# Kernel tuning notes

Measured on AMD Instinct MI355X. Metric: run time of the kernel, lower is better.

The kernel has to match this reference:

```python
import jax, jax.numpy as jnp
import numpy as np

N = 50000
E = 800000
HID = 32
HEADS = 8
OUT_DIM = 16
NEG_SLOPE = 0.2
LN_EPS = 1e-5


def setup_inputs() -> dict:
    key = jax.random.key(0)
    ks = jax.random.split(key, 32)
    rn = lambda k, shape, s=0.1: (jax.random.normal(k, shape, jnp.float32) * s)
    d = {}
    d['x'] = jax.random.normal(ks[0], (N, 1), jnp.float32)
    d['edge_index'] = jax.random.randint(ks[1], (2, E), 0, N, dtype=jnp.int64)
    d['batch'] = jnp.zeros((N,), dtype=jnp.int64)
    # in_layer: Linear(1, HID)
    d['Win'] = rn(ks[2], (1, HID)); d['bin_'] = rn(ks[3], (HID,))
    # layer 0: residual Linear(HID, HID*HEADS), GATConv(HID -> HID, heads=HEADS, concat)
    d['Wr0'] = rn(ks[4], (HID, HID * HEADS)); d['br0'] = rn(ks[5], (HID * HEADS,))
    d['W0'] = rn(ks[6], (HID, HID * HEADS))
    d['as0'] = rn(ks[7], (HEADS, HID)); d['ad0'] = rn(ks[8], (HEADS, HID))
    d['bg0'] = rn(ks[9], (HID * HEADS,))
    d['g0'] = jnp.ones((HID * HEADS,), jnp.float32); d['b0'] = jnp.zeros((HID * HEADS,), jnp.float32)
    # layer 1: residual Linear(HID*HEADS, HID), GATConv(HID*HEADS -> HID, heads=1, concat=False)
    d['Wr1'] = rn(ks[10], (HID * HEADS, HID)); d['br1'] = rn(ks[11], (HID,))
    d['W1'] = rn(ks[12], (HID * HEADS, HID))
    d['as1'] = rn(ks[13], (1, HID)); d['ad1'] = rn(ks[14], (1, HID))
    d['bg1'] = rn(ks[15], (HID,))
    d['g1'] = jnp.ones((HID,), jnp.float32); d['b1'] = jnp.zeros((HID,), jnp.float32)
    # out_layer: Linear(HID, OUT_DIM)
    d['Wout'] = rn(ks[16], (HID, OUT_DIM)); d['bout'] = rn(ks[17], (OUT_DIM,))
    return d


def _layer_norm(x, g, b):
    m = x.mean(-1, keepdims=True)
    v = ((x - m) ** 2).mean(-1, keepdims=True)
    return (x - m) * jax.lax.rsqrt(v + LN_EPS) * g + b


def _gat_conv(x, src, dst, W, att_src, att_dst, bias, heads, n):
    # x: [n, in]; W: [in, heads*out]; att_*: [heads, out]
    h = (x @ W).reshape(n, heads, -1)                      # [n, H, F]
    a_s = (h * att_src).sum(-1)                            # [n, H]
    a_d = (h * att_dst).sum(-1)                            # [n, H]
    e = jax.nn.leaky_relu(a_s[src] + a_d[dst], NEG_SLOPE)  # [E', H]
    emax = jax.ops.segment_max(e, dst, num_segments=n)
    ex = jnp.exp(e - emax[dst])
    denom = jax.ops.segment_sum(ex, dst, num_segments=n)
    alpha = ex / (denom[dst] + 1e-16)                      # segment softmax per dst node
    out = jax.ops.segment_sum(h[src] * alpha[..., None], dst, num_segments=n)  # [n, H, F]
    return out.reshape(n, -1) + bias                       # concat heads (heads=1 -> mean=identity)


def reference(x, edge_index, batch, Win, bin_, Wr0, br0, W0, as0, ad0, bg0, g0, b0,
              Wr1, br1, W1, as1, ad1, bg1, g1, b1, Wout, bout):
    n = x.shape[0]
    loop = jnp.arange(n, dtype=edge_index.dtype)
    src = jnp.concatenate([edge_index[0], loop])  # PyG GATConv add_self_loops=True
    dst = jnp.concatenate([edge_index[1], loop])

    h = x @ Win + bin_                                       # [n, HID]
    # layer 0
    res = h @ Wr0 + br0
    h = _gat_conv(h, src, dst, W0, as0, ad0, bg0, HEADS, n)  # [n, HID*HEADS]
    h = jax.nn.elu(h)                                        # not last layer
    h = _layer_norm(h + res, g0, b0)
    # layer 1 (last)
    res = h @ Wr1 + br1
    h = _gat_conv(h, src, dst, W1, as1, ad1, bg1, 1, n)      # [n, HID]
    h = _layer_norm(h + res, g1, b1)
    # global mean pool
    n_graphs = 1
    sums = jax.ops.segment_sum(h, batch, num_segments=n_graphs)
    cnts = jax.ops.segment_sum(jnp.ones((n, 1), h.dtype), batch, num_segments=n_graphs)
    pooled = sums / cnts                                     # [1, HID]
    return pooled @ Wout + bout                              # [1, OUT_DIM]
```

## Files before the change

### kernel.cpp

```cpp
#include <hip/hip_runtime.h>
#include <hip/hip_fp16.h>
#include <math.h>

#define N_NODES 50000
#define N_EDGES 800000
#define HEADS 8
#define OUTD 16
#define NEG_SLOPE 0.2f
#define LN_EPS 1e-5f
#define NB0 196
#define NEGBIG -3.0e38f
#define PADDEG 64
#define NPOOL 64
#define SC_CHUNK 2048
#define SC_NCHUNK ((N_EDGES + SC_CHUNK - 1) / SC_CHUNK)
#define NGRAN 3125
#define NBLK_REMAP 12512

typedef _Float16 half8 __attribute__((ext_vector_type(8)));
typedef float f32x4 __attribute__((ext_vector_type(4)));

__device__ __forceinline__ int remap_base(int b, bool& ok) {
    int p = b & 7, q = b >> 3;
    int c = (q >> 2) * 8 + p;
    ok = (c < NGRAN);
    return c * 16 + (q & 3) * 4;
}

__global__ __launch_bounds__(256) void k_prep(const float* __restrict__ Win,
    const float* __restrict__ bin, const float* __restrict__ Wr0,
    const float* __restrict__ br0, const float* __restrict__ W0,
    const float* __restrict__ as0, const float* __restrict__ ad0,
    float* __restrict__ tab, float* __restrict__ tabPQRS,
    int* __restrict__ cnt, float* __restrict__ partial) {
    const int t = threadIdx.x;
    const int tid = blockIdx.x * 256 + t;
    if (tid < N_NODES) cnt[tid] = 0;
    if (tid < NPOOL * 32) partial[tid] = 0.f;
    if (blockIdx.x != 0) return;
    __shared__ float sA1[256], sB1[256];
    float a0 = 0.f, b0 = 0.f, a1 = 0.f, b1 = 0.f;
#pragma unroll
    for (int k = 0; k < 32; k++) {
        float wk = Win[k], bk = bin[k];
        float wr = Wr0[k * 256 + t];
        float ww = W0[k * 256 + t];
        a0 = fmaf(wk, wr, a0); b0 = fmaf(bk, wr, b0);
        a1 = fmaf(wk, ww, a1); b1 = fmaf(bk, ww, b1);
    }
    b0 += br0[t];
    sA1[t] = a1; sB1[t] = b1;
    tab[t] = a0; tab[256 + t] = b0; tab[512 + t] = a1; tab[768 + t] = b1;
    __syncthreads();
    if (t < 8) {
        float P = 0.f, Q = 0.f, R = 0.f, S = 0.f;
        for (int c = 0; c < 32; c++) {
            float aw = sA1[t * 32 + c], bw = sB1[t * 32 + c];
            float av = as0[t * 32 + c], dv = ad0[t * 32 + c];
            P = fmaf(aw, av, P); Q = fmaf(bw, av, Q);
            R = fmaf(aw, dv, R); S = fmaf(bw, dv, S);
        }
        tabPQRS[t] = P; tabPQRS[8 + t] = Q; tabPQRS[16 + t] = R; tabPQRS[24 + t] = S;
    }
}

__global__ __launch_bounds__(256) void k_scatter(const int* __restrict__ srcA,
    const int* __restrict__ dstA, int* cnt, unsigned short* __restrict__ csrp) {
    const int phase = blockIdx.x & 7;
    const int chunk = blockIdx.x >> 3;
    const int base = chunk * SC_CHUNK + threadIdx.x;
#pragma unroll
    for (int k = 0; k < 8; k++) {
        int e = base + k * 256;
        if (e < N_EDGES) {
            int d = dstA[e];
            if (((d >> 4) & 7) == phase) {
                int p = atomicAdd(&cnt[d], 1);
                if (p < PADDEG - 1) csrp[d * PADDEG + p] = (unsigned short)srcA[e];
            }
        }
    }
}

__global__ __launch_bounds__(256) void k_agg0(const int* __restrict__ cnt,
    const unsigned short* __restrict__ csrp, const float* __restrict__ x,
    const float* __restrict__ tab, const float* __restrict__ tabPQRS,
    const float* __restrict__ bg0, const float* __restrict__ g0,
    const float* __restrict__ b0, __half* __restrict__ h1out) {
    bool ok;
    const int base = remap_base(blockIdx.x, ok);
    if (!ok) return;
    const int t = threadIdx.x;
    const int w = t >> 6, l = t & 63;
    const int i = base + w;
    const int slot = l >> 3, h = l & 7;
    const int row = i * PADDEG;
    const int total = min(cnt[i], PADDEG - 1) + 1;
    const float xi = x[i];
    float xsv[8];
    float xmn = 3.0e38f, xmx = -3.0e38f;
#pragma unroll
    for (int k = 0; k < 8; k++) {
        int idx = slot + k * 8;
        float xs = 0.f;
        if (idx < total) {
            int s = (idx == 0) ? i : (int)csrp[row + idx - 1];
            xs = x[s];
            xmn = fminf(xmn, xs);
            xmx = fmaxf(xmx, xs);
        }
        xsv[k] = xs;
    }
#pragma unroll
    for (int o = 1; o <= 32; o <<= 1) {
        xmn = fminf(xmn, __shfl_xor(xmn, o));
        xmx = fmaxf(xmx, __shfl_xor(xmx, o));
    }
    const float P = tabPQRS[h];
    const float C = tabPQRS[8 + h] + fmaf(xi, tabPQRS[16 + h], tabPQRS[24 + h]);
    float em = fmaf(P, (P >= 0.f) ? xmx : xmn, C);
    em = (em > 0.f) ? em : NEG_SLOPE * em;
    float psum = 0.f, pxsum = 0.f;
#pragma unroll
    for (int k = 0; k < 8; k++) {
        int idx = slot + k * 8;
        if (idx < total) {
            float e = fmaf(P, xsv[k], C);
            e = (e > 0.f) ? e : NEG_SLOPE * e;
            float p = __expf(e - em);
            psum += p;
            pxsum = fmaf(p, xsv[k], pxsum);
        }
    }
    psum += __shfl_xor(psum, 8);   pxsum += __shfl_xor(pxsum, 8);
    psum += __shfl_xor(psum, 16);  pxsum += __shfl_xor(pxsum, 16);
    psum += __shfl_xor(psum, 32);  pxsum += __shfl_xor(pxsum, 32);
    const int hl = l >> 3;
    const float Ph  = __shfl(psum, hl);
    const float PXh = __shfl(pxsum, hl);
    const float inv = 1.f / (Ph + 1e-16f);
    const float Xh = PXh * inv;
    const float Sh = Ph * inv;
    const int c = l * 4;
    float4 A0v = *(const float4*)(tab + c);
    float4 B0v = *(const float4*)(tab + 256 + c);
    float4 A1v = *(const float4*)(tab + 512 + c);
    float4 B1v = *(const float4*)(tab + 768 + c);
    float4 bg = *(const float4*)(bg0 + c);
    float val[4];
    val[0] = fmaf(A1v.x, Xh, fmaf(B1v.x, Sh, bg.x));
    val[1] = fmaf(A1v.y, Xh, fmaf(B1v.y, Sh, bg.y));
    val[2] = fmaf(A1v.z, Xh, fmaf(B1v.z, Sh, bg.z));
    val[3] = fmaf(A1v.w, Xh, fmaf(B1v.w, Sh, bg.w));
#pragma unroll
    for (int k = 0; k < 4; k++) val[k] = (val[k] > 0.f) ? val[k] : expm1f(val[k]);
    val[0] += fmaf(xi, A0v.x, B0v.x);
    val[1] += fmaf(xi, A0v.y, B0v.y);
    val[2] += fmaf(xi, A0v.z, B0v.z);
    val[3] += fmaf(xi, A0v.w, B0v.w);
    float sm = val[0] + val[1] + val[2] + val[3];
#pragma unroll
    for (int o = 1; o <= 32; o <<= 1) sm += __shfl_xor(sm, o);
    float mean = sm * (1.f / 256.f);
    float d[4], vv = 0.f;
#pragma unroll
    for (int k = 0; k < 4; k++) { d[k] = val[k] - mean; vv = fmaf(d[k], d[k], vv); }
#pragma unroll
    for (int o = 1; o <= 32; o <<= 1) vv += __shfl_xor(vv, o);
    float rstd = rsqrtf(vv * (1.f / 256.f) + LN_EPS);
    float4 gv = *(const float4*)(g0 + c);
    float4 bv = *(const float4*)(b0 + c);
    __half2 o0 = __float22half2_rn(make_float2(fmaf(d[0] * rstd, gv.x, bv.x),
                                               fmaf(d[1] * rstd, gv.y, bv.y)));
    __half2 o1 = __float22half2_rn(make_float2(fmaf(d[2] * rstd, gv.z, bv.z),
                                               fmaf(d[3] * rstd, gv.w, bv.w)));
    uint2 ou;
    ou.x = *(unsigned*)&o0; ou.y = *(unsigned*)&o1;
    *(uint2*)(h1out + (size_t)i * 256 + c) = ou;
}

__global__ __launch_bounds__(256) void k_lin1(const __half* __restrict__ h1h,
    const float* __restrict__ Wr1, const float* __restrict__ br1,
    const float* __restrict__ W1,  const float* __restrict__ as1,
    const float* __restrict__ ad1,
    __half* __restrict__ res1h, __half* __restrict__ hW1h,
    float* __restrict__ a_s1, float* __restrict__ a_d1) {
    const int t = threadIdx.x;
    __shared__ _Float16 Bs[16384];
    for (int idx = t; idx < 16384; idx += 256) {
        int j = idx & 7;
        int n = (idx >> 3) & 63;
        int qk = idx >> 9;
        int k = qk * 8 + j;
        float wv = (n < 32) ? Wr1[k * 32 + n] : W1[k * 32 + (n - 32)];
        Bs[idx] = (_Float16)wv;
    }
    __syncthreads();
    const int w = t >> 6, l = t & 63;
    const int q = l >> 4;
    const int nodeA = blockIdx.x * 64 + w * 16 + (l & 15);
    const half8* B8 = (const half8*)Bs;
    f32x4 c0 = {0.f, 0.f, 0.f, 0.f}, c1 = c0, c2 = c0, c3 = c0;
#pragma unroll
    for (int kt = 0; kt < 8; kt++) {
        half8 a = {0,0,0,0,0,0,0,0};
        if (nodeA < N_NODES)
            a = *(const half8*)(h1h + (size_t)nodeA * 256 + kt * 32 + q * 8);
        const int bb = (kt * 4 + q) * 64 + (l & 15);
        c0 = __builtin_amdgcn_mfma_f32_16x16x32_f16(a, B8[bb +  0], c0, 0, 0, 0);
        c1 = __builtin_amdgcn_mfma_f32_16x16x32_f16(a, B8[bb + 16], c1, 0, 0, 0);
        c2 = __builtin_amdgcn_mfma_f32_16x16x32_f16(a, B8[bb + 32], c2, 0, 0, 0);
        c3 = __builtin_amdgcn_mfma_f32_16x16x32_f16(a, B8[bb + 48], c3, 0, 0, 0);
    }
    const int col = l & 15;
    const int nodeE = blockIdx.x * 64 + w * 16 + q * 4;
    const float brv0 = br1[col], brv1 = br1[col + 16];
    const float asv0 = as1[col], asv1 = as1[col + 16];
    const float adv0 = ad1[col], adv1 = ad1[col + 16];
    float ps[4], pd[4];
#pragma unroll
    for (int r = 0; r < 4; r++) {
        int nd = nodeE + r;
        if (nd < N_NODES) {
            res1h[nd * 32 + col]      = __float2half(c0[r] + brv0);
            res1h[nd * 32 + col + 16] = __float2half(c1[r] + brv1);
            hW1h[nd * 32 + col]      = __float2half(c2[r]);
            hW1h[nd * 32 + col + 16] = __float2half(c3[r]);
        }
        ps[r] = c2[r] * asv0 + c3[r] * asv1;
        pd[r] = c2[r] * adv0 + c3[r] * adv1;
    }
#pragma unroll
    for (int o = 1; o <= 8; o <<= 1) {
#pragma unroll
        for (int r = 0; r < 4; r++) {
            ps[r] += __shfl_xor(ps[r], o);
            pd[r] += __shfl_xor(pd[r], o);
        }
    }
    if (col == 0) {
#pragma unroll
        for (int r = 0; r < 4; r++) {
            int nd = nodeE + r;
            if (nd < N_NODES) { a_s1[nd] = ps[r]; a_d1[nd] = pd[r]; }
        }
    }
}

__global__ __launch_bounds__(256) void k_agg1(const int* __restrict__ cnt,
    const unsigned short* __restrict__ csrp, const float* __restrict__ a_s1,
    const float* __restrict__ a_d1, const __half* __restrict__ hW1h,
    const float* __restrict__ bg1, const __half* __restrict__ res1h,
    const float* __restrict__ g1, const float* __restrict__ b1,
    float* __restrict__ partial) {
    bool ok;
    const int base = remap_base(blockIdx.x, ok);
    if (!ok) return;
    const int t = threadIdx.x;
    const int w = t >> 6, l = t & 63;
    const int i = base + w;
    const int row = i * PADDEG;
    const int total = min(cnt[i], PADDEG - 1) + 1;
    const float ad = a_d1[i];
    const bool valid = (l < total);
    int sl = i;
    if (valid && l > 0) sl = (int)csrp[row + l - 1];
    float e = NEGBIG;
    if (valid) {
        e = a_s1[sl] + ad;
        e = (e > 0.f) ? e : NEG_SLOPE * e;
    }
    float mx = e;
#pragma unroll
    for (int o = 1; o <= 32; o <<= 1) mx = fmaxf(mx, __shfl_xor(mx, o));
    float pl = valid ? __expf(e - mx) : 0.f;
    float lsum = pl;
#pragma unroll
    for (int o = 1; o <= 32; o <<= 1) lsum += __shfl_xor(lsum, o);
    const float inv = 1.f / (lsum + 1e-16f);
    const int slot = l >> 3, u = l & 7;
    float4 acc = make_float4(0.f, 0.f, 0.f, 0.f);
    for (int idx = slot; idx < total; idx += 8) {
        int s = __shfl(sl, idx);
        float p = __shfl(pl, idx);
        uint2 uu = *(const uint2*)(hW1h + (size_t)s * 32 + u * 4);
        float2 v0 = __half22float2(*(const __half2*)&uu.x);
        float2 v1 = __half22float2(*(const __half2*)&uu.y);
        acc.x = fmaf(p, v0.x, acc.x); acc.y = fmaf(p, v0.y, acc.y);
        acc.z = fmaf(p, v1.x, acc.z); acc.w = fmaf(p, v1.y, acc.w);
    }
#pragma unroll
    for (int o = 8; o <= 32; o <<= 1) {
        acc.x += __shfl_xor(acc.x, o); acc.y += __shfl_xor(acc.y, o);
        acc.z += __shfl_xor(acc.z, o); acc.w += __shfl_xor(acc.w, o);
    }
    float4 bg = *(const float4*)(bg1 + u * 4);
    uint2 ru = *(const uint2*)(res1h + (size_t)i * 32 + u * 4);
    float2 rr0 = __half22float2(*(const __half2*)&ru.x);
    float2 rr1 = __half22float2(*(const __half2*)&ru.y);
    float4 val;
    val.x = fmaf(acc.x, inv, bg.x) + rr0.x; val.y = fmaf(acc.y, inv, bg.y) + rr0.y;
    val.z = fmaf(acc.z, inv, bg.z) + rr1.x; val.w = fmaf(acc.w, inv, bg.w) + rr1.y;
    float sm = val.x + val.y + val.z + val.w;
    sm += __shfl_xor(sm, 1); sm += __shfl_xor(sm, 2); sm += __shfl_xor(sm, 4);
    float mean = sm * (1.f / 32.f);
    float4 d;
    d.x = val.x - mean; d.y = val.y - mean; d.z = val.z - mean; d.w = val.w - mean;
    float vv = d.x * d.x + d.y * d.y + d.z * d.z + d.w * d.w;
    vv += __shfl_xor(vv, 1); vv += __shfl_xor(vv, 2); vv += __shfl_xor(vv, 4);
    float rstd = rsqrtf(vv * (1.f / 32.f) + LN_EPS);
    float4 gv = *(const float4*)(g1 + u * 4);
    float4 bv = *(const float4*)(b1 + u * 4);
    float4 outv;
    outv.x = fmaf(d.x * rstd, gv.x, bv.x); outv.y = fmaf(d.y * rstd, gv.y, bv.y);
    outv.z = fmaf(d.z * rstd, gv.z, bv.z); outv.w = fmaf(d.w * rstd, gv.w, bv.w);
    __shared__ float sp[4][32];
    if (l < 8) *(float4*)(&sp[w][u * 4]) = outv;
    __syncthreads();
    if (t < 32) {
        float s = sp[0][t] + sp[1][t] + sp[2][t] + sp[3][t];
        atomicAdd(&partial[(blockIdx.x & (NPOOL - 1)) * 32 + t], s);
    }
}

__global__ __launch_bounds__(64) void k_final(const float* __restrict__ partial,
                                              const float* __restrict__ Wout,
                                              const float* __restrict__ bout,
                                              float* __restrict__ out) {
    __shared__ float pooled[32];
    int t = threadIdx.x;
    if (t < 32) {
        float a = 0.f;
        for (int b = 0; b < NPOOL; b++) a += partial[b * 32 + t];
        pooled[t] = a * (1.f / (float)N_NODES);
    }
    __syncthreads();
    if (t < OUTD) {
        float o = bout[t];
        for (int c = 0; c < 32; c++) o = fmaf(pooled[c], Wout[c * OUTD + t], o);
        out[t] = o;
    }
}

extern "C" void kernel_launch(void* const* d_in, const int* in_sizes, int n_in,
                              void* d_out, int out_size, void* d_ws, size_t ws_size,
                              hipStream_t stream) {
    const float* x    = (const float*)d_in[0];
    const int*   eidx = (const int*)d_in[1];
    const float* Win  = (const float*)d_in[3];
    const float* bin  = (const float*)d_in[4];
    const float* Wr0  = (const float*)d_in[5];
    const float* br0  = (const float*)d_in[6];
    const float* W0   = (const float*)d_in[7];
    const float* as0  = (const float*)d_in[8];
    const float* ad0  = (const float*)d_in[9];
    const float* bg0  = (const float*)d_in[10];
    const float* g0   = (const float*)d_in[11];
    const float* b0   = (const float*)d_in[12];
    const float* Wr1  = (const float*)d_in[13];
    const float* br1  = (const float*)d_in[14];
    const float* W1   = (const float*)d_in[15];
    const float* as1  = (const float*)d_in[16];
    const float* ad1  = (const float*)d_in[17];
    const float* bg1  = (const float*)d_in[18];
    const float* g1   = (const float*)d_in[19];
    const float* b1   = (const float*)d_in[20];
    const float* Wout = (const float*)d_in[21];
    const float* bout = (const float*)d_in[22];
    float* out = (float*)d_out;

    const int* srcA = eidx;
    const int* dstA = eidx + N_EDGES;

    char* B = (char*)d_ws;
    __half* h1h = (__half*)B;
    __half* res1h = (__half*)(B + 25600000);
    __half* hW1h = (__half*)(B + 29600000);
    float* a_s1  = (float*)(B + 33600000);
    float* a_d1  = (float*)(B + 33900000);
    unsigned short* csrp = (unsigned short*)(B + 34200000);
    int* cnt     = (int*)(B + 40600000);
    float* partial = (float*)(B + 40900000);
    float* tab   = (float*)(B + 40910000);
    float* tabPQRS = (float*)(B + 40915000);

    k_prep<<<NB0, 256, 0, stream>>>(Win, bin, Wr0, br0, W0, as0, ad0,
                                    tab, tabPQRS, cnt, partial);
    k_scatter<<<SC_NCHUNK * 8, 256, 0, stream>>>(srcA, dstA, cnt, csrp);
    k_agg0<<<NBLK_REMAP, 256, 0, stream>>>(cnt, csrp, x, tab, tabPQRS,
                                           bg0, g0, b0, h1h);
    k_lin1<<<(N_NODES + 63) / 64, 256, 0, stream>>>(h1h, Wr1, br1, W1, as1, ad1,
                                                    res1h, hW1h, a_s1, a_d1);
    k_agg1<<<NBLK_REMAP, 256, 0, stream>>>(cnt, csrp, a_s1, a_d1, hW1h,
                                           bg1, res1h, g1, b1, partial);
    k_final<<<1, 64, 0, stream>>>(partial, Wout, bout, out);
}
```

Baseline: 221.1 us.

## Prepack layer-1 weights once, vectorize scatter loads, trim shuffles and ELU

```diff
diff --git a/kernel.cpp b/kernel.cpp
--- a/kernel.cpp
+++ b/kernel.cpp
@@ -31,13 +31,25 @@
     const float* __restrict__ bin, const float* __restrict__ Wr0,
     const float* __restrict__ br0, const float* __restrict__ W0,
     const float* __restrict__ as0, const float* __restrict__ ad0,
+    const float* __restrict__ Wr1, const float* __restrict__ W1,
     float* __restrict__ tab, float* __restrict__ tabPQRS,
+    _Float16* __restrict__ wpk,
     int* __restrict__ cnt, float* __restrict__ partial) {
     const int t = threadIdx.x;
-    const int tid = blockIdx.x * 256 + t;
+    const int bx = blockIdx.x;
+    const int tid = bx * 256 + t;
     if (tid < N_NODES) cnt[tid] = 0;
     if (tid < NPOOL * 32) partial[tid] = 0.f;
-    if (blockIdx.x != 0) return;
+    if (bx >= 1 && bx <= 64) {
+        int idx = (bx - 1) * 256 + t;
+        int j = idx & 7;
+        int n = (idx >> 3) & 63;
+        int qk = idx >> 9;
+        int k = qk * 8 + j;
+        float wv = (n < 32) ? Wr1[k * 32 + n] : W1[k * 32 + (n - 32)];
+        wpk[idx] = (_Float16)wv;
+    }
+    if (bx != 0) return;
     __shared__ float sA1[256], sB1[256];
     float a0 = 0.f, b0 = 0.f, a1 = 0.f, b1 = 0.f;
 #pragma unroll
@@ -68,15 +80,22 @@
     const int* __restrict__ dstA, int* cnt, unsigned short* __restrict__ csrp) {
     const int phase = blockIdx.x & 7;
     const int chunk = blockIdx.x >> 3;
-    const int base = chunk * SC_CHUNK + threadIdx.x;
-#pragma unroll
-    for (int k = 0; k < 8; k++) {
-        int e = base + k * 256;
-        if (e < N_EDGES) {
-            int d = dstA[e];
-            if (((d >> 4) & 7) == phase) {
-                int p = atomicAdd(&cnt[d], 1);
-                if (p < PADDEG - 1) csrp[d * PADDEG + p] = (unsigned short)srcA[e];
+    const int4* __restrict__ d4p = (const int4*)dstA;
+    const int f0 = chunk * (SC_CHUNK / 4) + threadIdx.x;
+#pragma unroll
+    for (int k = 0; k < 2; k++) {
+        int f = f0 + k * 256;
+        int e0 = f * 4;
+        if (e0 < N_EDGES) {
+            int4 dv = d4p[f];
+            int dd[4] = {dv.x, dv.y, dv.z, dv.w};
+#pragma unroll
+            for (int u = 0; u < 4; u++) {
+                int d = dd[u];
+                if (((d >> 4) & 7) == phase) {
+                    int p = atomicAdd(&cnt[d], 1);
+                    if (p < PADDEG - 1) csrp[d * PADDEG + p] = (unsigned short)srcA[e0 + u];
+                }
             }
         }
     }
@@ -112,7 +131,7 @@
         xsv[k] = xs;
     }
 #pragma unroll
-    for (int o = 1; o <= 32; o <<= 1) {
+    for (int o = 8; o <= 32; o <<= 1) {
         xmn = fminf(xmn, __shfl_xor(xmn, o));
         xmx = fmaxf(xmx, __shfl_xor(xmx, o));
     }
@@ -153,7 +172,7 @@
     val[2] = fmaf(A1v.z, Xh, fmaf(B1v.z, Sh, bg.z));
     val[3] = fmaf(A1v.w, Xh, fmaf(B1v.w, Sh, bg.w));
 #pragma unroll
-    for (int k = 0; k < 4; k++) val[k] = (val[k] > 0.f) ? val[k] : expm1f(val[k]);
+    for (int k = 0; k < 4; k++) val[k] = (val[k] > 0.f) ? val[k] : (__expf(val[k]) - 1.f);
     val[0] += fmaf(xi, A0v.x, B0v.x);
     val[1] += fmaf(xi, A0v.y, B0v.y);
     val[2] += fmaf(xi, A0v.z, B0v.z);
@@ -180,39 +199,32 @@
 }
 
 __global__ __launch_bounds__(256) void k_lin1(const __half* __restrict__ h1h,
-    const float* __restrict__ Wr1, const float* __restrict__ br1,
-    const float* __restrict__ W1,  const float* __restrict__ as1,
-    const float* __restrict__ ad1,
+    const _Float16* __restrict__ wpk, const float* __restrict__ br1,
+    const float* __restrict__ as1, const float* __restrict__ ad1,
     __half* __restrict__ res1h, __half* __restrict__ hW1h,
     float* __restrict__ a_s1, float* __restrict__ a_d1) {
     const int t = threadIdx.x;
-    __shared__ _Float16 Bs[16384];
-    for (int idx = t; idx < 16384; idx += 256) {
-        int j = idx & 7;
-        int n = (idx >> 3) & 63;
-        int qk = idx >> 9;
-        int k = qk * 8 + j;
-        float wv = (n < 32) ? Wr1[k * 32 + n] : W1[k * 32 + (n - 32)];
-        Bs[idx] = (_Float16)wv;
-    }
-    __syncthreads();
     const int w = t >> 6, l = t & 63;
     const int q = l >> 4;
-    const int nodeA = blockIdx.x * 64 + w * 16 + (l & 15);
-    const half8* B8 = (const half8*)Bs;
+    const int col = l & 15;
+    const int nodeA = blockIdx.x * 64 + w * 16 + col;
+    const half8* __restrict__ Bg = (const half8*)wpk;
     f32x4 c0 = {0.f, 0.f, 0.f, 0.f}, c1 = c0, c2 = c0, c3 = c0;
 #pragma unroll
     for (int kt = 0; kt < 8; kt++) {
         half8 a = {0,0,0,0,0,0,0,0};
         if (nodeA < N_NODES)
             a = *(const half8*)(h1h + (size_t)nodeA * 256 + kt * 32 + q * 8);
-        const int bb = (kt * 4 + q) * 64 + (l & 15);
-        c0 = __builtin_amdgcn_mfma_f32_16x16x32_f16(a, B8[bb +  0], c0, 0, 0, 0);
-        c1 = __builtin_amdgcn_mfma_f32_16x16x32_f16(a, B8[bb + 16], c1, 0, 0, 0);
-        c2 = __builtin_amdgcn_mfma_f32_16x16x32_f16(a, B8[bb + 32], c2, 0, 0, 0);
-        c3 = __builtin_amdgcn_mfma_f32_16x16x32_f16(a, B8[bb + 48], c3, 0, 0, 0);
-    }
-    const int col = l & 15;
+        const int bb = (kt * 4 + q) * 64 + col;
+        half8 b0 = Bg[bb +  0];
+        half8 b1 = Bg[bb + 16];
+        half8 b2 = Bg[bb + 32];
+        half8 b3 = Bg[bb + 48];
+        c0 = __builtin_amdgcn_mfma_f32_16x16x32_f16(a, b0, c0, 0, 0, 0);
+        c1 = __builtin_amdgcn_mfma_f32_16x16x32_f16(a, b1, c1, 0, 0, 0);
+        c2 = __builtin_amdgcn_mfma_f32_16x16x32_f16(a, b2, c2, 0, 0, 0);
+        c3 = __builtin_amdgcn_mfma_f32_16x16x32_f16(a, b3, c3, 0, 0, 0);
+    }
     const int nodeE = blockIdx.x * 64 + w * 16 + q * 4;
     const float brv0 = br1[col], brv1 = br1[col + 16];
     const float asv0 = as1[col], asv1 = as1[col + 16];
@@ -375,6 +387,7 @@
     char* B = (char*)d_ws;
     __half* h1h = (__half*)B;
     __half* res1h = (__half*)(B + 25600000);
+    _Float16* wpk = (_Float16*)(B + 28900000);
     __half* hW1h = (__half*)(B + 29600000);
     float* a_s1  = (float*)(B + 33600000);
     float* a_d1  = (float*)(B + 33900000);
@@ -384,12 +397,12 @@
     float* tab   = (float*)(B + 40910000);
     float* tabPQRS = (float*)(B + 40915000);
 
-    k_prep<<<NB0, 256, 0, stream>>>(Win, bin, Wr0, br0, W0, as0, ad0,
-                                    tab, tabPQRS, cnt, partial);
+    k_prep<<<NB0, 256, 0, stream>>>(Win, bin, Wr0, br0, W0, as0, ad0, Wr1, W1,
+                                    tab, tabPQRS, wpk, cnt, partial);
     k_scatter<<<SC_NCHUNK * 8, 256, 0, stream>>>(srcA, dstA, cnt, csrp);
     k_agg0<<<NBLK_REMAP, 256, 0, stream>>>(cnt, csrp, x, tab, tabPQRS,
                                            bg0, g0, b0, h1h);
-    k_lin1<<<(N_NODES + 63) / 64, 256, 0, stream>>>(h1h, Wr1, br1, W1, as1, ad1,
+    k_lin1<<<(N_NODES + 63) / 64, 256, 0, stream>>>(h1h, wpk, br1, as1, ad1,
                                                     res1h, hW1h, a_s1, a_d1);
     k_agg1<<<NBLK_REMAP, 256, 0, stream>>>(cnt, csrp, a_s1, a_d1, hW1h,
                                            bg1, res1h, g1, b1, partial);
```

New measurement: 210.4 us. -4.8%, faster.
